# Optimization experiments

Hardware: AMD Instinct MI355X
Metric: run time of the kernel (lower is better)

Reference implementation:

```python
import jax, jax.numpy as jnp
import numpy as np

B, T, D, V, U = 16, 1000, 512, 5000, 64


def _safe_logaddexp(a, b):
    # logaddexp with nan-safe gradients when both args are -inf
    both = jnp.isneginf(a) & jnp.isneginf(b)
    a_ = jnp.where(both, 0.0, a)
    b_ = jnp.where(both, 0.0, b)
    return jnp.where(both, -jnp.inf, jnp.logaddexp(a_, b_))


def _log_sub_exp(a, b):
    # faithful port of log_substraction_exp: log(exp(a) - exp(b)), stable
    mask1 = (~jnp.isinf(a)) & (~jnp.isinf(b))
    a_ = jnp.where(mask1, a, -1.0)
    b_ = jnp.where(mask1, b, -2.0)
    ans_tmp = b_ + jnp.log(jnp.exp(a_ - b_) - 1.0)
    a_ = jnp.where(jnp.isinf(ans_tmp), -2000.0, a_)
    b_ = jnp.where(jnp.isinf(ans_tmp), -2001.0, b_)
    ans1 = b_ + jnp.log(jnp.exp(a_ - b_) - 1.0)
    ans = jnp.where(mask1, ans1, -jnp.inf)
    mask2 = (~jnp.isinf(a)) & jnp.isinf(b)
    return jnp.where(mask2, a, ans)


def _ctc_trellis(logp, ys):
    # Standard CTC lattice over extended labels (blank interleaved), S = 2U+1.
    # alpha[t,b,s]: logprob of paths over frames 0..t ending in state s (incl. emission at t)
    # beta[t,b,s]:  logprob of emitting frames t+1..T-1 and finishing, given state s at t
    # This reproduces the k2 lattice forward/backward scores at the label states.
    Bb, Tt, _ = logp.shape
    Uu = ys.shape[1]
    S = 2 * Uu + 1
    l_ext = jnp.zeros((Bb, S), ys.dtype).at[:, 1::2].set(ys)  # blank=0 at even s
    lp = jnp.take_along_axis(logp, jnp.broadcast_to(l_ext[:, None, :], (Bb, Tt, S)), axis=2)
    skip_ok = jnp.zeros((Bb, S), bool).at[:, 3::2].set(ys[:, 1:] != ys[:, :-1])
    lpT = jnp.transpose(lp, (1, 0, 2))  # [T,B,S]
    ninf1 = jnp.full((Bb, 1), -jnp.inf)
    ninf2 = jnp.full((Bb, 2), -jnp.inf)

    a0 = jnp.full((Bb, S), -jnp.inf).at[:, :2].set(lpT[0, :, :2])

    def astep(ap, lp_t):
        s1 = jnp.concatenate([ninf1, ap[:, :-1]], 1)
        s2 = jnp.concatenate([ninf2, ap[:, :-2]], 1)
        a = lp_t + _safe_logaddexp(_safe_logaddexp(ap, s1), jnp.where(skip_ok, s2, -jnp.inf))
        return a, a

    _, arest = jax.lax.scan(astep, a0, lpT[1:])
    alpha = jnp.concatenate([a0[None], arest], 0)  # [T,B,S]

    bl = jnp.full((Bb, S), -jnp.inf).at[:, S - 2:].set(0.0)  # final states: last label / last blank
    skipL2 = jnp.concatenate([skip_ok[:, 2:], jnp.zeros((Bb, 2), bool)], 1)

    def bstep(bn, lp_next):
        m = lp_next + bn
        m1 = jnp.concatenate([m[:, 1:], ninf1], 1)
        m2 = jnp.concatenate([m[:, 2:], ninf2], 1)
        bcur = _safe_logaddexp(_safe_logaddexp(m, m1), jnp.where(skipL2, m2, -jnp.inf))
        return bcur, bcur

    _, brest = jax.lax.scan(bstep, bl, lpT[1:], reverse=True)
    beta = jnp.concatenate([brest, bl[None]], 0)  # [T,B,S]
    return alpha, beta, lp


def setup_inputs() -> dict:
    key = jax.random.key(0)
    k1, k2, k3 = jax.random.split(key, 3)
    hs_pad = jax.random.normal(k1, (B, T, D), jnp.float32)
    hlens = jnp.full((B,), T, jnp.int32)
    ys_pad = jax.random.randint(k2, (B, U), 1, V)  # labels in [1, V); 0 is blank
    ali = jnp.zeros((B, U), jnp.int32)  # unused when risk_factor == 0
    W = jax.random.normal(k3, (D, V), jnp.float32) * 0.02
    b = jnp.zeros((V,), jnp.float32)
    return {"hs_pad": hs_pad, "hlens": hlens, "ys_pad": ys_pad, "ali": ali, "W": W, "b": b}


def reference(hs_pad, hlens, ys_pad, ali, W, b):
    # ctc_lo + log_softmax (dropout_rate=0). hlens are all equal -> sort/unsort is identity.
    logp = jax.nn.log_softmax(hs_pad @ W + b, axis=-1)  # [B,T,V]
    alpha_f, beta_f, lp = _ctc_trellis(logp, ys_pad)
    alpha = jnp.transpose(alpha_f[:, :, 1::2], (1, 2, 0))  # [B,U,T]
    beta = jnp.transpose(beta_f[:, :, 1::2], (1, 2, 0))    # [B,U,T]
    p = jnp.transpose(lp[:, :, 1::2], (0, 2, 1))           # [B,U,T] logprob of label u at frame t
    # beta', excluding re-emission of label u at t+1 -> paths whose label-u segment ends at t
    bp = _log_sub_exp(beta[:, :, :-1], beta[:, :, 1:] + p[:, :, 1:])
    bp = jnp.concatenate([bp, beta[:, :, -1:]], -1)
    loss_state = alpha + bp
    loss_state = jnp.where(jnp.isnan(loss_state), -jnp.inf, loss_state)
    loss_u = jax.nn.logsumexp(loss_state, axis=2)  # aggregate == 'time'
    mask = jnp.isinf(loss_u)
    denom = (~mask).astype(loss_u.dtype).sum(1)
    loss_fsas = jnp.where(mask, 0.0, loss_u).sum(1) / denom
    Uu = ys_pad.shape[1]
    loss_fsas = jnp.where(hlens < Uu, 0.0, loss_fsas)
    return (-loss_fsas).mean()
```

## Files before the change

### kernel.cpp

```cpp
#include <hip/hip_runtime.h>

#define NB 16
#define NT 1000
#define ND 512
#define NV 5000
#define NVP 5120
#define NU 64
#define NLL 66
#define NM (NB * NT)
#define NCH 40

typedef short short8v __attribute__((ext_vector_type(8)));
typedef float float4v __attribute__((ext_vector_type(4)));

#define NEGINF (-__builtin_inff())
#define SENTL  (-1.0e30f)
#define LOG2E 1.4426950408889634f
#define LN2F  0.6931471805599453f
#define SENT2 (-2000.4586751f * LOG2E)

__device__ __forceinline__ float fexp2(float x) { return __builtin_amdgcn_exp2f(x); }
__device__ __forceinline__ float flog2(float x) { return __builtin_amdgcn_logf(x); }

__device__ __forceinline__ float dpp_shl1(float x) {
  int xi = __builtin_bit_cast(int, x);
  int r = __builtin_amdgcn_update_dpp(xi, xi, 0x130, 0xf, 0xf, false);
  return __builtin_bit_cast(float, r);
}
__device__ __forceinline__ float dpp_shr1(float x) {
  int xi = __builtin_bit_cast(int, x);
  int r = __builtin_amdgcn_update_dpp(xi, xi, 0x138, 0xf, 0xf, false);
  return __builtin_bit_cast(float, r);
}

__device__ __forceinline__ short f2bf(float x) {
  unsigned int u = __builtin_bit_cast(unsigned int, x);
  unsigned int r = (u + 0x7fffu + ((u >> 16) & 1u)) >> 16;
  return (short)(unsigned short)r;
}
__device__ __forceinline__ float bf2f(short h) {
  unsigned int u = ((unsigned int)(unsigned short)h) << 16;
  return __builtin_bit_cast(float, u);
}

__device__ __forceinline__ void g2lds16(const short* g, short* l) {
  __builtin_amdgcn_global_load_lds(
      (const __attribute__((address_space(1))) void*)g,
      (__attribute__((address_space(3))) void*)l, 16, 0, 0);
}

__device__ __forceinline__ float lae2s(float a, float b) {
  float m = fmaxf(a, b);
  return m + flog2(fexp2(a - m) + fexp2(b - m));
}
__device__ __forceinline__ float lae3s(float a, float b, float c) {
  float m = fmaxf(fmaxf(a, b), c);
  return m + flog2(fexp2(a - m) + fexp2(b - m) + fexp2(c - m));
}
__device__ __forceinline__ float lsub2(float a, float b) {
  if (b < -1.0e29f) return (a < -1.0e29f) ? SENTL : a;
  float tmp = b + flog2(fexp2(a - b) - 1.0f);
  if (__builtin_isinf(tmp)) tmp = SENT2;
  return tmp;
}

__global__ __launch_bounds__(256) void k_cvt(const float* __restrict__ hs,
                                             const float* __restrict__ W,
                                             short* __restrict__ hsb,
                                             short* __restrict__ WT,
                                             short* __restrict__ WTlo,
                                             float* __restrict__ outv) {
  __shared__ short tileH[64 * 72];
  __shared__ short tileL[64 * 72];
  if (blockIdx.x < 4000) {
    if (blockIdx.x == 0 && threadIdx.x == 0) outv[0] = 0.0f;
    size_t i = (size_t)blockIdx.x * 256 + threadIdx.x;
    const float4* p = (const float4*)hs + i * 2;
    float4 v0 = p[0], v1 = p[1];
    short8v r;
    r[0] = f2bf(v0.x); r[1] = f2bf(v0.y); r[2] = f2bf(v0.z); r[3] = f2bf(v0.w);
    r[4] = f2bf(v1.x); r[5] = f2bf(v1.y); r[6] = f2bf(v1.z); r[7] = f2bf(v1.w);
    int row = (int)(i >> 6);
    int g = (int)(i & 63);
    int gs = (g & ~7) | ((g & 7) ^ (row & 7));
    *(short8v*)(hsb + (size_t)row * ND + gs * 8) = r;
    return;
  }
  int bx = blockIdx.x - 4000;
  int n0 = (bx % 80) * 64, k0 = (bx / 80) * 64;
  int tid = threadIdx.x;
  int kr = tid >> 2, part = tid & 3;
  const float* src = W + (size_t)(k0 + kr) * NV + n0 + part * 16;
#pragma unroll
  for (int jj = 0; jj < 4; ++jj) {
    int c = n0 + part * 16 + jj * 4;
    float4 v;
    if (c + 3 < NV) {
      v = *(const float4*)(src + jj * 4);
    } else {
      v.x = (c + 0 < NV) ? src[jj * 4 + 0] : 0.f;
      v.y = (c + 1 < NV) ? src[jj * 4 + 1] : 0.f;
      v.z = (c + 2 < NV) ? src[jj * 4 + 2] : 0.f;
      v.w = (c + 3 < NV) ? src[jj * 4 + 3] : 0.f;
    }
    int base = kr * 72 + part * 16 + jj * 4;
    float vv[4] = {v.x, v.y, v.z, v.w};
#pragma unroll
    for (int q = 0; q < 4; ++q) {
      short h = f2bf(vv[q]);
      tileH[base + q] = h;
      tileL[base + q] = f2bf(vv[q] - bf2f(h));
    }
  }
  __syncthreads();
  int n = tid & 63, kq = tid >> 6;
  int nn = n0 + n;
  if (nn < NVP) {
#pragma unroll
    for (int half = 0; half < 2; ++half) {
      short8v vh, vl;
#pragma unroll
      for (int jj = 0; jj < 8; ++jj) {
        vh[jj] = tileH[(kq * 16 + half * 8 + jj) * 72 + n];
        vl[jj] = tileL[(kq * 16 + half * 8 + jj) * 72 + n];
      }
      int g = (k0 >> 3) + kq * 2 + half;
      int gs = (g & ~7) | ((g & 7) ^ (nn & 7));
      *(short8v*)(WT + (size_t)nn * ND + gs * 8) = vh;
      *(short8v*)(WTlo + (size_t)nn * ND + gs * 8) = vl;
    }
  }
}

__global__ __launch_bounds__(256) void k_labg(const short* __restrict__ hsb,
                                              const short* __restrict__ WT,
                                              const short* __restrict__ WTlo,
                                              const int* __restrict__ ys,
                                              const float* __restrict__ bias,
                                              float* __restrict__ ll) {
  __shared__ short As[128 * 64];
  __shared__ short Bh[128 * 64];
  __shared__ short Bl[128 * 64];

  int mt = blockIdx.x, b = blockIdx.y;
  int t0 = mt * 128;
  int tid = threadIdx.x;
  int lane = tid & 63, wave = tid >> 6;
  int wm = wave >> 1, wn = wave & 1;
  int lrow = lane & 15, lkhi = lane >> 4;

  const short* gaBase = hsb + (size_t)(b * NT + t0 + wave * 32 + (lane >> 3)) * ND + (lane & 7) * 8;

  int labv[4], xorv[4];
#pragma unroll
  for (int i = 0; i < 4; ++i) {
    int r = wave * 32 + (lane >> 3) + i * 8;
    int lab = (r == 0) ? 0 : ((r <= NU) ? ys[b * NU + r - 1] : NV);
    labv[i] = lab;
    xorv[i] = ((lane & 7) ^ (r & 7) ^ (lab & 7)) * 8;
  }

  float4v acc[4][4];
#pragma unroll
  for (int m = 0; m < 4; ++m)
#pragma unroll
    for (int n = 0; n < 4; ++n)
#pragma unroll
      for (int j = 0; j < 4; ++j) acc[m][n][j] = 0.f;

  for (int s = 0; s < 8; ++s) {
    int k0 = s * 64;
#pragma unroll
    for (int i = 0; i < 4; ++i) {
      g2lds16(gaBase + (size_t)(i * 8) * ND + k0, &As[(wave * 32 + i * 8) * 64]);
      g2lds16(WT + (size_t)labv[i] * ND + k0 + xorv[i], &Bh[(wave * 32 + i * 8) * 64]);
      g2lds16(WTlo + (size_t)labv[i] * ND + k0 + xorv[i], &Bl[(wave * 32 + i * 8) * 64]);
    }
    __syncthreads();
#pragma unroll
    for (int kk = 0; kk < 2; ++kk) {
      short8v av[4], bhv[4], blv2[4];
#pragma unroll
      for (int m = 0; m < 4; ++m) {
        int r = wm * 64 + m * 16 + lrow;
        int col = (kk * 32 + lkhi * 8) ^ ((r & 7) << 3);
        av[m] = *(const short8v*)&As[r * 64 + col];
      }
#pragma unroll
      for (int n = 0; n < 4; ++n) {
        int r = wn * 64 + n * 16 + lrow;
        int col = (kk * 32 + lkhi * 8) ^ ((r & 7) << 3);
        bhv[n] = *(const short8v*)&Bh[r * 64 + col];
        blv2[n] = *(const short8v*)&Bl[r * 64 + col];
      }
#pragma unroll
      for (int m = 0; m < 4; ++m)
#pragma unroll
        for (int n = 0; n < 4; ++n) {
          acc[m][n] = __builtin_amdgcn_mfma_f32_16x16x32_bf16(av[m], bhv[n], acc[m][n], 0, 0, 0);
          acc[m][n] = __builtin_amdgcn_mfma_f32_16x16x32_bf16(av[m], blv2[n], acc[m][n], 0, 0, 0);
        }
    }
    __syncthreads();
  }

  float bu[4]; bool uval[4];
#pragma unroll
  for (int n = 0; n < 4; ++n) {
    int u = wn * 64 + n * 16 + lrow;
    uval[n] = u < NU + 1;
    int lab = (u == 0) ? 0 : (uval[n] ? ys[b * NU + u - 1] : 0);
    bu[n] = uval[n] ? bias[lab] : 0.f;
  }
#pragma unroll
  for (int m = 0; m < 4; ++m)
#pragma unroll
    for (int j = 0; j < 4; ++j) {
      int trow = t0 + wm * 64 + m * 16 + lkhi * 4 + j;
      if (trow < NT) {
#pragma unroll
        for (int n = 0; n < 4; ++n) {
          int u = wn * 64 + n * 16 + lrow;
          if (uval[n])
            ll[((size_t)(b * NLL + u)) * NT + trow] = acc[m][n][j] + bu[n];
        }
      }
    }
}

__global__ __launch_bounds__(256) void k_big(const short* __restrict__ hsb,
                                             const short* __restrict__ WT,
                                             const float* __restrict__ bias,
                                             const float* __restrict__ ll,
                                             const int* __restrict__ ys,
                                             float* __restrict__ L,
                                             float* __restrict__ aod) {
  __shared__ short As[2][128 * 64];
  __shared__ short Ws[2][128 * 64];
  __shared__ float mred[128][2];
  __shared__ float sred[128][2];

  int bid = blockIdx.x;
  int tid = threadIdx.x;

  if (bid < NB) {
    float* pbS = (float*)As;
    int b = bid;
    const float* llb = ll + (size_t)b * NLL * NT;
    for (int i = tid; i < NT; i += 256) pbS[i] = llb[i] * LOG2E;
    __syncthreads();
    if (tid >= 64) return;
    int l = tid;
    const float* lrow = llb + (size_t)(1 + l) * NT;

    int lab = ys[b * NU + l];
    int labp = ys[b * NU + ((l >= 1) ? (l - 1) : 0)];
    bool skip = (l >= 1) && (lab != labp);
    float* aodb = aod + (size_t)b * NT * NU;

    float ae = (l == 0) ? pbS[0] : SENTL;
    float ao = (l == 0) ? lrow[0] * LOG2E : SENTL;
    aodb[l] = ao;

    float cl[16], pbr[16];
#pragma unroll
    for (int j = 0; j < 16; ++j) {
      int tt = 1 + j; if (tt > NT - 1) tt = NT - 1;
      cl[j] = lrow[tt];
      pbr[j] = pbS[tt];
    }
    for (int g = 0; g < 63; ++g) {
      float nl[16], pb2[16];
      if (g < 62) {
#pragma unroll
        for (int j = 0; j < 16; ++j) {
          int tt = 17 + g * 16 + j; if (tt > NT - 1) tt = NT - 1;
          nl[j] = lrow[tt];
          pb2[j] = pbS[tt];
        }
      } else {
#pragma unroll
        for (int j = 0; j < 16; ++j) { nl[j] = 0.f; pb2[j] = 0.f; }
      }
#pragma unroll
      for (int j = 0; j < 16; ++j) {
        int t = 1 + g * 16 + j;
        if (t < NT) {
          float pb = pbr[j];
          float pl = cl[j] * LOG2E;
          float po = dpp_shr1(ao); if (l == 0) po = SENTL;
          float aen = pb + lae2s(ae, po);
          float aon = pl + lae3s(ao, ae, skip ? po : SENTL);
          ae = aen; ao = aon;
          aodb[t * NU + l] = ao;
        }
      }
#pragma unroll
      for (int j = 0; j < 16; ++j) { cl[j] = nl[j]; pbr[j] = pb2[j]; }
    }
    return;
  }

  int lin = bid - NB;
  int o = (lin & 7) * 625 + (lin >> 3);
  int mt, chunk;
  if (o < 4800) {
    int sb = o / 320, w = o % 320;
    mt = sb * 8 + (w & 7);
    chunk = w >> 3;
  } else {
    int w = o - 4800;
    mt = 120 + (w % 5);
    chunk = w / 5;
  }
  int t0 = mt * 128;
  int n0 = chunk * 128;
  int lane = tid & 63, wave = tid >> 6;
  int wm = wave >> 1, wn = wave & 1;
  int lrow = lane & 15, lkhi = lane >> 4;

  const short* gaBase = hsb + (size_t)(t0 + wave * 32 + (lane >> 3)) * ND + (lane & 7) * 8;
  const short* gwBase = WT + (size_t)(n0 + wave * 32 + (lane >> 3)) * ND + (lane & 7) * 8;

  float4v acc[4][4];
#pragma unroll
  for (int m = 0; m < 4; ++m)
#pragma unroll
    for (int n = 0; n < 4; ++n)
#pragma unroll
      for (int j = 0; j < 4; ++j) acc[m][n][j] = 0.f;

  auto stage = [&](int s, int bw) {
    int k0 = s * 64;
#pragma unroll
    for (int i = 0; i < 4; ++i) {
      g2lds16(gaBase + (size_t)(i * 8) * ND + k0, &As[bw][(wave * 32 + i * 8) * 64]);
      g2lds16(gwBase + (size_t)(i * 8) * ND + k0, &Ws[bw][(wave * 32 + i * 8) * 64]);
    }
  };
  auto compute = [&](int bw) {
#pragma unroll
    for (int kk = 0; kk < 2; ++kk) {
      short8v av[4], wv[4];
#pragma unroll
      for (int m = 0; m < 4; ++m) {
        int r = wm * 64 + m * 16 + lrow;
        int col = (kk * 32 + lkhi * 8) ^ ((r & 7) << 3);
        av[m] = *(const short8v*)&As[bw][r * 64 + col];
      }
#pragma unroll
      for (int n = 0; n < 4; ++n) {
        int r = wn * 64 + n * 16 + lrow;
        int col = (kk * 32 + lkhi * 8) ^ ((r & 7) << 3);
        wv[n] = *(const short8v*)&Ws[bw][r * 64 + col];
      }
#pragma unroll
      for (int m = 0; m < 4; ++m)
#pragma unroll
        for (int n = 0; n < 4; ++n)
          acc[m][n] = __builtin_amdgcn_mfma_f32_16x16x32_bf16(av[m], wv[n], acc[m][n], 0, 0, 0);
    }
  };

  stage(0, 0);
  for (int s = 0; s < 8; ++s) {
    if (s < 7) {
      stage(s + 1, (s + 1) & 1);
      asm volatile("s_waitcnt vmcnt(8)" ::: "memory");
    } else {
      asm volatile("s_waitcnt vmcnt(0)" ::: "memory");
    }
    __builtin_amdgcn_sched_barrier(0);
    __builtin_amdgcn_s_barrier();
    compute(s & 1);
    __builtin_amdgcn_sched_barrier(0);
    __builtin_amdgcn_s_barrier();
  }

  float bcol[4]; bool cval[4];
#pragma unroll
  for (int n = 0; n < 4; ++n) {
    int c = n0 + wn * 64 + n * 16 + lrow;
    cval[n] = c < NV;
    bcol[n] = cval[n] ? bias[c] : 0.f;
  }
#pragma unroll
  for (int m = 0; m < 4; ++m)
#pragma unroll
    for (int j = 0; j < 4; ++j) {
      float mx = NEGINF;
#pragma unroll
      for (int n = 0; n < 4; ++n) {
        float v = cval[n] ? acc[m][n][j] + bcol[n] : NEGINF;
        mx = fmaxf(mx, v);
      }
#pragma unroll
      for (int d = 1; d < 16; d <<= 1) mx = fmaxf(mx, __shfl_xor(mx, d));
      float mxc = fmaxf(mx, -3.0e38f);
      float p = 0.f;
#pragma unroll
      for (int n = 0; n < 4; ++n) {
        float v = cval[n] ? acc[m][n][j] + bcol[n] : NEGINF;
        p += __expf(v - mxc);
      }
#pragma unroll
      for (int d = 1; d < 16; d <<= 1) p += __shfl_xor(p, d);
      if (lrow == 0) {
        int rloc = wm * 64 + m * 16 + lkhi * 4 + j;
        mred[rloc][wn] = mx;
        sred[rloc][wn] = p;
      }
    }
  __syncthreads();
  if (tid < 128) {
    int row = t0 + tid;
    float m0 = mred[tid][0], m1 = mred[tid][1];
    float m = fmaxf(m0, m1);
    float ss = 0.f;
    if (m != NEGINF)
      ss = ((m0 == NEGINF) ? 0.f : sred[tid][0] * __expf(m0 - m))
         + ((m1 == NEGINF) ? 0.f : sred[tid][1] * __expf(m1 - m));
    float Lv = (m == NEGINF || ss <= 0.f) ? NEGINF : m + __logf(ss);
    L[(size_t)chunk * NM + row] = Lv;
  }
}

__global__ __launch_bounds__(256) void k_dred(const float* __restrict__ L,
                                              float* __restrict__ dnm) {
  int row = blockIdx.x * 256 + threadIdx.x;
  if (row >= NM) return;
  float m40 = NEGINF;
#pragma unroll
  for (int c = 0; c < NCH; ++c) m40 = fmaxf(m40, L[(size_t)c * NM + row]);
  float s = 0.f;
#pragma unroll
  for (int c = 0; c < NCH; ++c) {
    float Lc = L[(size_t)c * NM + row];
    if (Lc > -1.0e29f) s += __expf(Lc - m40);
  }
  dnm[row] = m40 + __logf(s);
}

__global__ __launch_bounds__(512) void k_bwd(const float* __restrict__ ll,
                                             const float* __restrict__ dnm,
                                             const int* __restrict__ ys,
                                             float* __restrict__ bp) {
  __shared__ float dnS[8][NT];
  __shared__ float pbS[8][NT];
  int wave = threadIdx.x >> 6;
  int l = threadIdx.x & 63;
  int b = blockIdx.x * 8 + wave;
  const float* llb = ll + (size_t)b * NLL * NT;
  const float* dnb = dnm + b * NT;
  for (int t = l; t < NT; t += 64) {
    float d = dnb[t];
    dnS[wave][t] = d;
    pbS[wave][t] = (llb[t] - d) * LOG2E;
  }
  __syncthreads();
  const float* lrow = llb + (size_t)(1 + l) * NT;

  int lab = ys[b * NU + l];
  int labn = ys[b * NU + ((l < NU - 1) ? (l + 1) : l)];
  bool skipn = (l < NU - 1) && (labn != lab);
  float* bpb = bp + (size_t)b * NT * NU;

  float bo = (l == NU - 1) ? 0.0f : SENTL;
  float be = SENTL;
  float b128 = 0.0f;
  bpb[(NT - 1) * NU + l] = bo;

  float cl[16], pbr[16], dnr[16];
#pragma unroll
  for (int j = 0; j < 16; ++j) {
    int tt = NT - 2 - j; if (tt < 0) tt = 0;
    cl[j] = lrow[tt + 1];
    pbr[j] = pbS[wave][tt + 1];
    dnr[j] = dnS[wave][tt + 1];
  }
  for (int g = 0; g < 63; ++g) {
    float nl2[16], pb2[16], dn2[16];
    if (g < 62) {
#pragma unroll
      for (int j = 0; j < 16; ++j) {
        int tt = NT - 2 - 16 * (g + 1) - j; if (tt < 0) tt = 0;
        nl2[j] = lrow[tt + 1];
        pb2[j] = pbS[wave][tt + 1];
        dn2[j] = dnS[wave][tt + 1];
      }
    } else {
#pragma unroll
      for (int j = 0; j < 16; ++j) { nl2[j] = 0.f; pb2[j] = 0.f; dn2[j] = 0.f; }
    }
#pragma unroll
    for (int j = 0; j < 16; ++j) {
      int t = NT - 2 - 16 * g - j;
      if (t >= 0) {
        float pbv = pbr[j];
        float plv = (cl[j] - dnr[j]) * LOG2E;
        float me = pbv + be;
        float mo = plv + bo;
        float m128 = pbv + b128;
        float ne = dpp_shl1(me); if (l == NU - 1) ne = m128;
        float no = dpp_shl1(mo); if (l == NU - 1) no = SENTL;
        float ben = lae2s(me, mo);
        float bon = lae3s(mo, ne, skipn ? no : SENTL);
        bpb[t * NU + l] = lsub2(bon, mo);
        be = ben; bo = bon; b128 = m128;
      }
    }
#pragma unroll
    for (int j = 0; j < 16; ++j) { cl[j] = nl2[j]; pbr[j] = pb2[j]; dnr[j] = dn2[j]; }
  }
}

__global__ __launch_bounds__(512) void k_loss(const float* __restrict__ aod,
                                              const float* __restrict__ bp,
                                              const float* __restrict__ dnm,
                                              const int* __restrict__ hlens,
                                              float* __restrict__ out) {
  __shared__ float denL[NT];
  __shared__ float Dpre[NT];
  __shared__ float choff[64];
  __shared__ float ms[8][64], ss[8][64];
  int b = blockIdx.x, tid = threadIdx.x;
  for (int t = tid; t < NT; t += 512) denL[t] = dnm[b * NT + t];
  __syncthreads();
  if (tid < 64) {
    float s = 0.f;
#pragma unroll
    for (int i = 0; i < 16; ++i) { int t = tid * 16 + i; if (t < NT) s += denL[t]; }
    float v = s;
#pragma unroll
    for (int d = 1; d < 64; d <<= 1) { float u = __shfl_up(v, d); if (tid >= d) v += u; }
    choff[tid] = v - s;
  }
  __syncthreads();
  for (int t = tid; t < NT; t += 512) {
    float s = choff[t >> 4];
    int base = t & ~15;
    for (int i = base; i <= t; ++i) s += denL[i];
    Dpre[t] = s;
  }
  __syncthreads();
  int w = tid >> 6, l = tid & 63;
  const float* ab = aod + (size_t)b * NT * NU;
  const float* pbp = bp + (size_t)b * NT * NU;
  float m = NEGINF, s = 0.f;
  int t0 = w * 125, t1 = t0 + 125;
  for (int t = t0; t < t1; ++t) {
    float av = ab[t * NU + l];
    float pv = pbp[t * NU + l];
    float x = av - Dpre[t] * LOG2E + pv;
    if (__builtin_isnan(x) || x < -1.0e29f) continue;
    if (x > m) { s = s * fexp2(m - x) + 1.0f; m = x; }
    else       { s += fexp2(x - m); }
  }
  ms[w][l] = m; ss[w][l] = s;
  __syncthreads();
  if (w == 0) {
    float mm = NEGINF;
#pragma unroll
    for (int i = 0; i < 8; ++i) mm = fmaxf(mm, ms[i][l]);
    float lu;
    if (mm == NEGINF) lu = NEGINF;
    else {
      float st = 0.f;
#pragma unroll
      for (int i = 0; i < 8; ++i)
        st += (ms[i][l] == NEGINF) ? 0.f : ss[i][l] * fexp2(ms[i][l] - mm);
      lu = (mm + flog2(st)) * LN2F;
    }
    bool msk = __builtin_isinf(lu);
    float sv = msk ? 0.f : lu;
    float cv = msk ? 0.f : 1.f;
#pragma unroll
    for (int d = 1; d < 64; d <<= 1) { sv += __shfl_xor(sv, d); cv += __shfl_xor(cv, d); }
    if (l == 0) {
      float lf = sv / cv;
      if (hlens[b] < NU) lf = 0.f;
      atomicAdd(out, -lf * (1.0f / NB));
    }
  }
}

extern "C" void kernel_launch(void* const* d_in, const int* in_sizes, int n_in,
                              void* d_out, int out_size, void* d_ws, size_t ws_size,
                              hipStream_t stream) {
  const float* hs    = (const float*)d_in[0];
  const int*   hlens = (const int*)d_in[1];
  const int*   ys    = (const int*)d_in[2];
  const float* W     = (const float*)d_in[4];
  const float* bias  = (const float*)d_in[5];
  float* out = (float*)d_out;

  char* ws = (char*)d_ws;
  short* hsb   = (short*)(ws + 0);
  short* WT    = (short*)(ws + 16384000);
  short* WTlo  = (short*)(ws + 21626880);
  float* aod   = (float*)(ws + 21626880);
  float* ll    = (float*)(ws + 26869760);
  float* L     = (float*)(ws + 31093760);
  float* dnm   = (float*)(ws + 33653760);
  float* bpb   = (float*)(ws + 33717760);

  k_cvt<<<4640, 256, 0, stream>>>(hs, W, hsb, WT, WTlo, out);
  k_labg<<<dim3(8, 16), 256, 0, stream>>>(hsb, WT, WTlo, ys, bias, ll);
  k_big<<<5016, 256, 0, stream>>>(hsb, WT, bias, ll, ys, L, aod);
  k_dred<<<63, 256, 0, stream>>>(L, dnm);
  k_bwd<<<2, 512, 0, stream>>>(ll, dnm, ys, bpb);
  k_loss<<<16, 512, 0, stream>>>(aod, bpb, dnm, hlens, out);
}
```

Measured before the change: 447.5 us.

## Vectorize CTC recurrence loads and spread backward pass across sixteen blocks

The forward alpha recurrence and the backward beta recurrence now load label-row and blank/denominator values as aligned float4 vectors, in 16-frame chunks. The loop bounds are peeled so the per-step bounds check and clamp go away. The backward kernel moves from 2 blocks of 8 waves to 16 single-wave blocks, one per batch item. This lets the latency-bound sequential scans run on separate CUs instead of sharing two. The risk is that the float4 loads depend on 16-byte alignment of the row offsets, since each row is NT=1000 floats.

```diff
diff --git a/kernel.cpp b/kernel.cpp
--- a/kernel.cpp
+++ b/kernel.cpp
@@ -262,42 +262,47 @@
     float ao = (l == 0) ? lrow[0] * LOG2E : SENTL;
     aodb[l] = ao;
 
-    float cl[16], pbr[16];
-#pragma unroll
-    for (int j = 0; j < 16; ++j) {
-      int tt = 1 + j; if (tt > NT - 1) tt = NT - 1;
-      cl[j] = lrow[tt];
-      pbr[j] = pbS[tt];
-    }
-    for (int g = 0; g < 63; ++g) {
-      float nl[16], pb2[16];
-      if (g < 62) {
-#pragma unroll
-        for (int j = 0; j < 16; ++j) {
-          int tt = 17 + g * 16 + j; if (tt > NT - 1) tt = NT - 1;
-          nl[j] = lrow[tt];
-          pb2[j] = pbS[tt];
-        }
-      } else {
-#pragma unroll
-        for (int j = 0; j < 16; ++j) { nl[j] = 0.f; pb2[j] = 0.f; }
-      }
-#pragma unroll
-      for (int j = 0; j < 16; ++j) {
-        int t = 1 + g * 16 + j;
-        if (t < NT) {
-          float pb = pbr[j];
-          float pl = cl[j] * LOG2E;
-          float po = dpp_shr1(ao); if (l == 0) po = SENTL;
-          float aen = pb + lae2s(ae, po);
-          float aon = pl + lae3s(ao, ae, skip ? po : SENTL);
-          ae = aen; ao = aon;
-          aodb[t * NU + l] = ao;
-        }
-      }
-#pragma unroll
-      for (int j = 0; j < 16; ++j) { cl[j] = nl[j]; pbr[j] = pb2[j]; }
-    }
+#define STEPF(T, CLV, PBV)                                         \
+    {                                                              \
+      float pl_ = (CLV) * LOG2E;                                   \
+      float po_ = dpp_shr1(ao); if (l == 0) po_ = SENTL;           \
+      float aen_ = (PBV) + lae2s(ae, po_);                         \
+      float aon_ = pl_ + lae3s(ao, ae, skip ? po_ : SENTL);        \
+      ae = aen_; ao = aon_;                                        \
+      aodb[(T) * NU + l] = ao;                                     \
+    }
+
+    float4v h4[4], hp4[4], c4[4], p4[4];
+#pragma unroll
+    for (int q = 0; q < 4; ++q) {
+      h4[q] = *(const float4v*)&lrow[q * 4];
+      hp4[q] = *(const float4v*)&pbS[q * 4];
+      c4[q] = *(const float4v*)&lrow[16 + q * 4];
+      p4[q] = *(const float4v*)&pbS[16 + q * 4];
+    }
+#pragma unroll
+    for (int j = 0; j < 15; ++j) {
+      int e = 1 + j;
+      STEPF(1 + j, h4[e >> 2][e & 3], hp4[e >> 2][e & 3]);
+    }
+    for (int m = 1; m <= 61; ++m) {
+      float4v n4[4], np4[4];
+      int nb = (m < 61) ? (m + 1) * 16 : 992;
+#pragma unroll
+      for (int q = 0; q < 4; ++q) {
+        n4[q] = *(const float4v*)&lrow[nb + q * 4];
+        np4[q] = *(const float4v*)&pbS[nb + q * 4];
+      }
+#pragma unroll
+      for (int j = 0; j < 16; ++j)
+        STEPF(16 * m + j, c4[j >> 2][j & 3], p4[j >> 2][j & 3]);
+#pragma unroll
+      for (int q = 0; q < 4; ++q) { c4[q] = n4[q]; p4[q] = np4[q]; }
+    }
+#pragma unroll
+    for (int j = 0; j < 8; ++j)
+      STEPF(992 + j, c4[j >> 2][j & 3], p4[j >> 2][j & 3]);
+#undef STEPF
     return;
   }
 
@@ -441,21 +446,20 @@
   dnm[row] = m40 + __logf(s);
 }
 
-__global__ __launch_bounds__(512) void k_bwd(const float* __restrict__ ll,
-                                             const float* __restrict__ dnm,
-                                             const int* __restrict__ ys,
-                                             float* __restrict__ bp) {
-  __shared__ float dnS[8][NT];
-  __shared__ float pbS[8][NT];
-  int wave = threadIdx.x >> 6;
-  int l = threadIdx.x & 63;
-  int b = blockIdx.x * 8 + wave;
+__global__ __launch_bounds__(64) void k_bwd(const float* __restrict__ ll,
+                                            const float* __restrict__ dnm,
+                                            const int* __restrict__ ys,
+                                            float* __restrict__ bp) {
+  __shared__ float dnS[1024];
+  __shared__ float pbS[1024];
+  int b = blockIdx.x;
+  int l = threadIdx.x;
   const float* llb = ll + (size_t)b * NLL * NT;
   const float* dnb = dnm + b * NT;
   for (int t = l; t < NT; t += 64) {
     float d = dnb[t];
-    dnS[wave][t] = d;
-    pbS[wave][t] = (llb[t] - d) * LOG2E;
+    dnS[t] = d;
+    pbS[t] = (llb[t] - d) * LOG2E;
   }
   __syncthreads();
   const float* lrow = llb + (size_t)(1 + l) * NT;
@@ -470,48 +474,58 @@
   float b128 = 0.0f;
   bpb[(NT - 1) * NU + l] = bo;
 
-  float cl[16], pbr[16], dnr[16];
-#pragma unroll
-  for (int j = 0; j < 16; ++j) {
-    int tt = NT - 2 - j; if (tt < 0) tt = 0;
-    cl[j] = lrow[tt + 1];
-    pbr[j] = pbS[wave][tt + 1];
-    dnr[j] = dnS[wave][tt + 1];
-  }
-  for (int g = 0; g < 63; ++g) {
-    float nl2[16], pb2[16], dn2[16];
-    if (g < 62) {
-#pragma unroll
-      for (int j = 0; j < 16; ++j) {
-        int tt = NT - 2 - 16 * (g + 1) - j; if (tt < 0) tt = 0;
-        nl2[j] = lrow[tt + 1];
-        pb2[j] = pbS[wave][tt + 1];
-        dn2[j] = dnS[wave][tt + 1];
-      }
-    } else {
-#pragma unroll
-      for (int j = 0; j < 16; ++j) { nl2[j] = 0.f; pb2[j] = 0.f; dn2[j] = 0.f; }
+#define STEPB(T, CLV, PBV, DNV)                                    \
+  {                                                                \
+    float plv_ = ((CLV) - (DNV)) * LOG2E;                          \
+    float me_ = (PBV) + be;                                        \
+    float mo_ = plv_ + bo;                                         \
+    float m128_ = (PBV) + b128;                                    \
+    float ne_ = dpp_shl1(me_); if (l == NU - 1) ne_ = m128_;       \
+    float no_ = dpp_shl1(mo_); if (l == NU - 1) no_ = SENTL;       \
+    float ben_ = lae2s(me_, mo_);                                  \
+    float bon_ = lae3s(mo_, ne_, skipn ? no_ : SENTL);             \
+    bpb[(T) * NU + l] = lsub2(bon_, mo_);                          \
+    be = ben_; bo = bon_; b128 = m128_;                            \
+  }
+
+  float4v h4[4], hp4[4], hd4[4], c4[4], p4[4], d4[4];
+#pragma unroll
+  for (int q = 0; q < 4; ++q) {
+    h4[q] = *(const float4v*)&lrow[992 + q * 4];
+    hp4[q] = *(const float4v*)&pbS[992 + q * 4];
+    hd4[q] = *(const float4v*)&dnS[992 + q * 4];
+    c4[q] = *(const float4v*)&lrow[976 + q * 4];
+    p4[q] = *(const float4v*)&pbS[976 + q * 4];
+    d4[q] = *(const float4v*)&dnS[976 + q * 4];
+  }
+#pragma unroll
+  for (int j = 0; j < 8; ++j) {
+    int e = 7 - j;
+    STEPB(998 - j, h4[e >> 2][e & 3], hp4[e >> 2][e & 3], hd4[e >> 2][e & 3]);
+  }
+  for (int m = 61; m >= 1; --m) {
+    float4v n4[4], np4[4], nd4[4];
+    int nb = (m > 1) ? (m - 1) * 16 : 0;
+#pragma unroll
+    for (int q = 0; q < 4; ++q) {
+      n4[q] = *(const float4v*)&lrow[nb + q * 4];
+      np4[q] = *(const float4v*)&pbS[nb + q * 4];
+      nd4[q] = *(const float4v*)&dnS[nb + q * 4];
     }
 #pragma unroll
     for (int j = 0; j < 16; ++j) {
-      int t = NT - 2 - 16 * g - j;
-      if (t >= 0) {
-        float pbv = pbr[j];
-        float plv = (cl[j] - dnr[j]) * LOG2E;
-        float me = pbv + be;
-        float mo = plv + bo;
-        float m128 = pbv + b128;
-        float ne = dpp_shl1(me); if (l == NU - 1) ne = m128;
-        float no = dpp_shl1(mo); if (l == NU - 1) no = SENTL;
-        float ben = lae2s(me, mo);
-        float bon = lae3s(mo, ne, skipn ? no : SENTL);
-        bpb[t * NU + l] = lsub2(bon, mo);
-        be = ben; bo = bon; b128 = m128;
-      }
-    }
-#pragma unroll
-    for (int j = 0; j < 16; ++j) { cl[j] = nl2[j]; pbr[j] = pb2[j]; dnr[j] = dn2[j]; }
-  }
+      int e = 15 - j;
+      STEPB(16 * m + 14 - j, c4[e >> 2][e & 3], p4[e >> 2][e & 3], d4[e >> 2][e & 3]);
+    }
+#pragma unroll
+    for (int q = 0; q < 4; ++q) { c4[q] = n4[q]; p4[q] = np4[q]; d4[q] = nd4[q]; }
+  }
+#pragma unroll
+  for (int j = 0; j < 15; ++j) {
+    int e = 15 - j;
+    STEPB(14 - j, c4[e >> 2][e & 3], p4[e >> 2][e & 3], d4[e >> 2][e & 3]);
+  }
+#undef STEPB
 }
 
 __global__ __launch_bounds__(512) void k_loss(const float* __restrict__ aod,
@@ -608,6 +622,6 @@
   k_labg<<<dim3(8, 16), 256, 0, stream>>>(hsb, WT, WTlo, ys, bias, ll);
   k_big<<<5016, 256, 0, stream>>>(hsb, WT, bias, ll, ys, L, aod);
   k_dred<<<63, 256, 0, stream>>>(L, dnm);
-  k_bwd<<<2, 512, 0, stream>>>(ll, dnm, ys, bpb);
+  k_bwd<<<16, 64, 0, stream>>>(ll, dnm, ys, bpb);
   k_loss<<<16, 512, 0, stream>>>(aod, bpb, dnm, hlens, out);
 }
```

New measurement: 384.2 us. 1.16x faster.
